# Optimization experiments

Measured on AMD Instinct MI355X. Metric: run time of the kernel, lower is better.

Reference implementation:

```python
import jax, jax.numpy as jnp
import numpy as np

K_MAX = 30


def setup_inputs() -> dict:
    key = jax.random.key(0)
    ks = jax.random.split(key, 4)
    b, N, f0, f1, f2 = 8, 256, 512, 256, 128
    x = jax.random.normal(ks[0], (b, N, f0), dtype=jnp.float32)
    W0 = jax.random.normal(ks[1], (f0, f1), dtype=jnp.float32) / np.sqrt(f0).astype(np.float32)
    b0 = jnp.zeros((f1,), jnp.float32)
    W1 = jax.random.normal(ks[2], (f1, f2), dtype=jnp.float32) / np.sqrt(f1).astype(np.float32)
    b1 = jnp.zeros((f2,), jnp.float32)
    return {"x": x, "W0": W0, "b0": b0, "W1": W1, "b1": b1}


def _dist(x, W0, b0, W1, b1):
    # DIST: 2-layer MLP (ReLU after layer 0 only), then cosine distance matrix
    h = jax.nn.relu(x @ W0 + b0)
    z = h @ W1 + b1                                   # [b,N,f2]
    corr = jnp.einsum('bnd,bmd->bnm', z, z)           # [b,N,N]
    d = jnp.diagonal(corr, axis1=1, axis2=2)          # [b,N] squared norms
    denom = jnp.sqrt(jnp.clip(d[:, :, None] * d[:, None, :], 1e-8))
    return (1.0 - corr / denom) / 2.0


def _d_sum(D):
    # D_SUM_CALC: D_sum[n,m] = sum of D over block [min(n,m)..max(n,m)]^2,
    # except the -1 subdiagonal which stays D[n, n-1] (torch code path).
    b, N, _ = D.shape
    P = jnp.pad(jnp.cumsum(jnp.cumsum(D, axis=1), axis=2), ((0, 0), (1, 0), (1, 0)))
    n = jnp.arange(N)
    lo = jnp.minimum(n[:, None], n[None, :])
    hi = jnp.maximum(n[:, None], n[None, :])
    block = P[:, hi + 1, hi + 1] - P[:, lo, hi + 1] - P[:, hi + 1, lo] + P[:, lo, lo]
    sub = (n[:, None] - n[None, :]) == 1              # row = col+1
    return jnp.where(sub, D, block)


def _c_table(D_sum, K):
    # C_TABLE_ALL: sequential DP over kk, vectorized over (nn, ii) and batch.
    b, N, _ = D_sum.shape
    nn = jnp.arange(N)[:, None]
    ii = jnp.arange(N)[None, :]
    CA0 = jnp.full((b, N, N), -1.0, dtype=D_sum.dtype).at[:, :, N - 1].set(1.0)
    C_prev = D_sum[:, :, N - 1]                       # C[:, :, 0]
    CA = [CA0]
    for kk in range(1, K):
        # temp[nn, ii] = D_sum[nn, ii] + C[ii+1, kk-1],  nn <= ii < N-kk
        Cshift = jnp.pad(C_prev[:, 1:], ((0, 0), (0, 1)))
        T = D_sum + Cshift[:, None, :]                # [b,N,N]
        valid = (ii >= nn) & (ii < N - kk)            # [N,N]
        sm = jax.nn.softmax(jnp.where(valid, -T, -1e30), axis=-1)  # softmin
        CA.append(jnp.where(valid, sm, -1.0))
        Cmin = jnp.min(jnp.where(valid, T, 1e30), axis=-1)         # [b,N]
        C_prev = jnp.where(jnp.arange(N) < N - kk, Cmin, 0.0)
    return jnp.stack(CA, axis=2)                      # [b,N,K,N]


def reference(x, W0, b0, W1, b1):
    D = _dist(x, W0, b0, W1, b1)
    Ds = _d_sum(D)
    C_all = _c_table(Ds, K_MAX)
    mask = (C_all >= 0).astype(C_all.dtype)
    return (C_all * mask).sum((1, 2)) / mask.sum((1, 2))   # [b,N]
```

## Files before the change

kernel.cpp:

```cpp
#include <hip/hip_runtime.h>

constexpr int NB    = 8;
constexpr int NN    = 256;
constexpr int F0    = 512;
constexpr int F1    = 256;
constexpr int F2    = 128;
constexpr int ROWS  = NB * NN;
constexpr int KMAX  = 30;
constexpr float INF = 1e30f;

__global__ __launch_bounds__(256) void gemm_bias_act(
    const float* __restrict__ A, const float* __restrict__ B,
    const float* __restrict__ bias, float* __restrict__ C,
    int M, int Ncols, int K, int relu)
{
  __shared__ float As[16][64];
  __shared__ float Bs[16][32];
  const int tid = threadIdx.x;
  const int tx = tid & 15;
  const int ty = tid >> 4;
  const int rowBase = blockIdx.y * 64;
  const int colBase = blockIdx.x * 32;
  float acc[4][2] = {};
  for (int k0 = 0; k0 < K; k0 += 16) {
    {
      const int r  = tid >> 2;
      const int kq = (tid & 3) << 2;
      const float4 av = *(const float4*)(A + (size_t)(rowBase + r) * K + (k0 + kq));
      As[kq+0][r] = av.x; As[kq+1][r] = av.y; As[kq+2][r] = av.z; As[kq+3][r] = av.w;
      const int kr = tid >> 4;
      const int c2 = (tid & 15) << 1;
      const float2 bv = *(const float2*)(B + (size_t)(k0 + kr) * Ncols + (colBase + c2));
      Bs[kr][c2+0] = bv.x; Bs[kr][c2+1] = bv.y;
    }
    __syncthreads();
    #pragma unroll
    for (int kk = 0; kk < 16; kk++) {
      const float4 a = *(const float4*)&As[kk][ty*4];
      const float b0v = Bs[kk][tx*2+0];
      const float b1v = Bs[kk][tx*2+1];
      acc[0][0] += a.x*b0v; acc[0][1] += a.x*b1v;
      acc[1][0] += a.y*b0v; acc[1][1] += a.y*b1v;
      acc[2][0] += a.z*b0v; acc[2][1] += a.z*b1v;
      acc[3][0] += a.w*b0v; acc[3][1] += a.w*b1v;
    }
    __syncthreads();
  }
  #pragma unroll
  for (int i = 0; i < 4; i++) {
    const int rr = rowBase + ty*4 + i;
    #pragma unroll
    for (int j = 0; j < 2; j++) {
      const int cc = colBase + tx*2 + j;
      float v = acc[i][j] + bias[cc];
      if (relu) v = fmaxf(v, 0.0f);
      C[(size_t)rr * Ncols + cc] = v;
    }
  }
}

__global__ __launch_bounds__(256) void corr_dist(
    const float* __restrict__ z, float* __restrict__ D)
{
  const int b = blockIdx.z;
  const float* zb = z + (size_t)b * NN * F2;
  __shared__ float As[16][64];
  __shared__ float Bs[16][64];
  const int tid = threadIdx.x;
  const int tx = tid & 15;
  const int ty = tid >> 4;
  const int rowBase = blockIdx.y * 64;
  const int colBase = blockIdx.x * 64;
  float acc[4][4] = {};
  float nsr[4] = {}, nsc[4] = {};
  for (int k0 = 0; k0 < F2; k0 += 16) {
    {
      const int r  = tid >> 2;
      const int kq = (tid & 3) << 2;
      const float4 av = *(const float4*)(zb + (size_t)(rowBase + r) * F2 + (k0 + kq));
      As[kq+0][r] = av.x; As[kq+1][r] = av.y; As[kq+2][r] = av.z; As[kq+3][r] = av.w;
      const float4 bv = *(const float4*)(zb + (size_t)(colBase + r) * F2 + (k0 + kq));
      Bs[kq+0][r] = bv.x; Bs[kq+1][r] = bv.y; Bs[kq+2][r] = bv.z; Bs[kq+3][r] = bv.w;
    }
    __syncthreads();
    #pragma unroll
    for (int kk = 0; kk < 16; kk++) {
      const float4 a = *(const float4*)&As[kk][ty*4];
      const float4 bq = *(const float4*)&Bs[kk][tx*4];
      const float ar[4] = {a.x, a.y, a.z, a.w};
      const float br[4] = {bq.x, bq.y, bq.z, bq.w};
      #pragma unroll
      for (int i = 0; i < 4; i++) { nsr[i] += ar[i]*ar[i]; nsc[i] += br[i]*br[i]; }
      #pragma unroll
      for (int i = 0; i < 4; i++)
        #pragma unroll
        for (int j = 0; j < 4; j++)
          acc[i][j] += ar[i] * br[j];
    }
    __syncthreads();
  }
  float* Db = D + (size_t)b * NN * NN;
  #pragma unroll
  for (int i = 0; i < 4; i++) {
    const int rr = rowBase + ty*4 + i;
    #pragma unroll
    for (int j = 0; j < 4; j++) {
      const int cc = colBase + tx*4 + j;
      const float denom = sqrtf(fmaxf(nsr[i] * nsc[j], 1e-8f));
      Db[(size_t)rr * NN + cc] = 0.5f * (1.0f - acc[i][j] / denom);
    }
  }
}

__global__ __launch_bounds__(256) void scan_slab(
    const float* __restrict__ D, double* __restrict__ S, double* __restrict__ aux)
{
  const int s = blockIdx.x & 7;
  const int b = blockIdx.x >> 3;
  const int tid = threadIdx.x;
  const int wave = tid >> 6, lane = tid & 63;
  __shared__ double sd[32][NN];
  for (int t = 0; t < 8; t++) {
    const int rl = wave * 8 + t;
    const float4 dv = *(const float4*)(D + (size_t)(b * NN + s * 32 + rl) * NN + lane * 4);
    double d0 = dv.x, d1 = dv.y, d2 = dv.z, d3 = dv.w;
    double p0 = d0, p1 = p0 + d1, p2 = p1 + d2, p3 = p2 + d3;
    double tt = p3;
    #pragma unroll
    for (int d = 1; d < 64; d <<= 1) {
      double u = __shfl_up(tt, d);
      if (lane >= d) tt += u;
    }
    const double off = tt - p3;
    sd[rl][lane*4+0] = off + p0; sd[rl][lane*4+1] = off + p1;
    sd[rl][lane*4+2] = off + p2; sd[rl][lane*4+3] = off + p3;
  }
  __syncthreads();
  const int j = tid;
  double* Sp = S + (size_t)b * NN * NN + (size_t)(s * 32) * NN + j;
  double sum = 0.0;
  for (int r = 0; r < 32; r += 8) {
    double v0 = sd[r+0][j], v1 = sd[r+1][j], v2 = sd[r+2][j], v3 = sd[r+3][j];
    double v4 = sd[r+4][j], v5 = sd[r+5][j], v6 = sd[r+6][j], v7 = sd[r+7][j];
    v0 += sum; v1 += v0; v2 += v1; v3 += v2; v4 += v3; v5 += v4; v6 += v5; v7 += v6;
    Sp[(size_t)(r+0)*NN] = v0; Sp[(size_t)(r+1)*NN] = v1;
    Sp[(size_t)(r+2)*NN] = v2; Sp[(size_t)(r+3)*NN] = v3;
    Sp[(size_t)(r+4)*NN] = v4; Sp[(size_t)(r+5)*NN] = v5;
    Sp[(size_t)(r+6)*NN] = v6; Sp[(size_t)(r+7)*NN] = v7;
    sum = v7;
  }
  aux[((size_t)b * 8 + s) * NN + j] = sum;
}

__global__ __launch_bounds__(256) void ds_mat(
    const double* __restrict__ S, const double* __restrict__ aux,
    float* __restrict__ A, float* __restrict__ Cstk, float* __restrict__ out)
{
  const int slab = blockIdx.x;
  const int b = blockIdx.y;
  const double* Sb = S + (size_t)b * NN * NN;
  float* Ab = A + (size_t)b * NN * NN;
  const int tid = threadIdx.x;
  const int w = tid >> 6, lane = tid & 63;
  __shared__ double P[8][NN];
  __shared__ double diag[NN];
  {
    const double* ax = aux + (size_t)b * 8 * NN + tid;
    double run = 0.0;
    #pragma unroll
    for (int u = 0; u < 8; u++) { P[u][tid] = run; run += ax[(size_t)u * NN]; }
  }
  __syncthreads();
  diag[tid] = Sb[(size_t)tid * NN + tid] + P[tid >> 5][tid];
  __syncthreads();
  #pragma unroll
  for (int t = 0; t < 4; t++) {
    const int n = slab * 16 + w * 4 + t;
    const double snn = (n > 0) ? diag[n-1] : 0.0;
    const double* srow = Sb + (size_t)(n > 0 ? n-1 : 0) * NN;
    const double* Pr   = P[(n > 0 ? n-1 : 0) >> 5];
    #pragma unroll
    for (int c = 0; c < 4; c++) {
      const int jx = c * 64 + lane;
      float ds = INF;
      if (jx >= n) {
        const double sv = (n > 0) ? (srow[jx] + Pr[jx]) : 0.0;
        ds = (float)(diag[jx] - 2.0 * sv + snn);
      }
      if (jx < NN - 1) Ab[(size_t)n * NN + jx + 1] = ds;
      else             Cstk[(size_t)b * 32 * NN + n] = ds;
      if (jx == 0)     Ab[(size_t)n * NN + 0] = INF;
    }
  }
  if (slab == 0) out[b * NN + tid] = (tid == NN - 1) ? 1.0f : 0.0f;
}

constexpr int CSTR = 260;
constexpr int RING = 8;

__global__ __launch_bounds__(1024) void chain_full(
    const float* __restrict__ A, float* __restrict__ Cstk)
{
  const int b = blockIdx.x;
  const int tid = threadIdx.x;
  const int n = tid >> 2, q = tid & 3;
  __shared__ __align__(16) float cs[RING * CSTR];
  float* Ck = Cstk + (size_t)b * 32 * NN;
  const size_t mb = (size_t)b * NN * NN;

  const int jj0 = (n + 1) & ~3;
  const int La  = NN - jj0;

  float4 areg[16];
  {
    const float* ar = A + mb + (size_t)n * NN + jj0;
    #pragma unroll
    for (int fi = 0; fi < 16; fi++) {
      const int f = 4 * q + 16 * fi;
      if (f < La) areg[fi] = *(const float4*)(ar + f);
      else        areg[fi] = make_float4(INF, INF, INF, INF);
    }
  }

  if (tid < NN) cs[tid] = Ck[tid];
  __syncthreads();

  for (int t = 0; t < 29; t++) {
    float m = INF;
    const float* cb = cs + (t & (RING-1)) * CSTR + jj0 + 4 * q;
    #pragma unroll
    for (int fi = 0; fi < 16; fi++) {
      const int f = 4 * q + 16 * fi;
      if (f < La) {
        const float4 a = areg[fi];
        const float4 c = *(const float4*)(cb + 16 * fi);
        m = fminf(m, fminf(fminf(a.x + c.x, a.y + c.y),
                           fminf(a.z + c.z, a.w + c.w)));
      }
    }
    m = fminf(m, __shfl_xor(m, 1));
    m = fminf(m, __shfl_xor(m, 2));
    m = fminf(m, INF);
    if (q == 0) {
      cs[((t + 1) & (RING-1)) * CSTR + n] = m;
      Ck[(t + 1) * NN + n] = m;
    }
    __syncthreads();
  }
}

__global__ __launch_bounds__(256) void sm_fused(
    const float* __restrict__ A, const float* __restrict__ Cstk,
    float* __restrict__ out)
{
  const int k = blockIdx.x + 1;
  const int b = blockIdx.y;
  const int limit = NN - k;
  const int tid = threadIdx.x;
  const float* Ab  = A + (size_t)b * NN * NN;
  const float* Ckb = Cstk + (size_t)b * 32 * NN;
  __shared__ __align__(16) float cprev[NN];
  __shared__ float ck[NN];
  __shared__ float ivh[NN];
  cprev[tid] = Ckb[(k - 1) * NN + tid];
  ck[tid]    = Ckb[k * NN + tid];
  __syncthreads();
  const int r = tid >> 2, q = tid & 3;
  #pragma unroll
  for (int rg = 0; rg < 4; rg++) {
    const int n = rg * 64 + r;
    const float m = ck[n];
    const float* Ar = Ab + (size_t)n * NN + q * 64;
    float s = 0.f;
    if (q * 64 + 63 > n) {
      #pragma unroll 4
      for (int i = 0; i < 16; i++) {
        const float4 a = *(const float4*)(Ar + i * 4);
        const int jj = q * 64 + i * 4;
        const float4 c = *(const float4*)&cprev[jj];
        s += (jj + 0 <= limit) ? __expf(m - a.x - c.x) : 0.f;
        s += (jj + 1 <= limit) ? __expf(m - a.y - c.y) : 0.f;
        s += (jj + 2 <= limit) ? __expf(m - a.z - c.z) : 0.f;
        s += (jj + 3 <= limit) ? __expf(m - a.w - c.w) : 0.f;
      }
    }
    s += __shfl_xor(s, 1);
    s += __shfl_xor(s, 2);
    if (q == 0) ivh[n] = 1.0f / s;
  }
  __syncthreads();
  const int j = tid;
  if (j < limit) {
    const float cj = cprev[j + 1];
    const int nmax = (j < limit - 1) ? j : limit - 1;
    float a = 0.0f;
    #pragma unroll 4
    for (int nr = 0; nr <= nmax; nr++)
      a += __expf(ck[nr] - Ab[(size_t)nr * NN + j + 1] - cj) * ivh[nr];
    int kmaxj = NN - 1 - j; if (kmaxj > KMAX - 1) kmaxj = KMAX - 1;
    const float cnt = (float)((j + 1) * kmaxj);
    atomicAdd(&out[b * NN + j], a / cnt);
  }
}

extern "C" void kernel_launch(void* const* d_in, const int* in_sizes, int n_in,
                              void* d_out, int out_size, void* d_ws, size_t ws_size,
                              hipStream_t stream) {
  const float* x  = (const float*)d_in[0];
  const float* W0 = (const float*)d_in[1];
  const float* b0 = (const float*)d_in[2];
  const float* W1 = (const float*)d_in[3];
  const float* b1 = (const float*)d_in[4];
  float* out = (float*)d_out;

  char* base = (char*)d_ws;
  float*  h    = (float*)(base);
  double* S    = (double*)(base);
  float*  D    = (float*)(base + (4u << 20));
  float*  A    = (float*)(base + (4u << 20));
  float*  z    = (float*)(base + (6u << 20));
  float*  Cstk = (float*)(base + (6u << 20));
  double* aux  = (double*)(base + (7u << 20));

  gemm_bias_act<<<dim3(F1/32, ROWS/64), 256, 0, stream>>>(x, W0, b0, h, ROWS, F1, F0, 1);
  gemm_bias_act<<<dim3(F2/32, ROWS/64), 256, 0, stream>>>(h, W1, b1, z, ROWS, F2, F1, 0);
  corr_dist<<<dim3(NN/64, NN/64, NB), 256, 0, stream>>>(z, D);
  scan_slab<<<dim3(NB*8), 256, 0, stream>>>(D, S, aux);
  ds_mat<<<dim3(16, NB), 256, 0, stream>>>(S, aux, A, Cstk, out);
  chain_full<<<dim3(NB), 1024, 0, stream>>>(A, Cstk);
  sm_fused<<<dim3(KMAX-1, NB), 256, 0, stream>>>(A, Cstk, out);
}
```

Baseline: 186.1 us.

## Fuse D_sum matrix construction into the DP chain kernel

Merges the ds_mat kernel into chain_full so each of the 8 batch blocks computes its own D_sum row entries from the prefix-sum data straight into registers, and still writes A out for the later softmin kernel. This drops one launch and the global round-trip that reloaded A before the DP. In exchange, the D_sum work runs on only 8 blocks instead of 128, so that part gets much less parallelism, and the scattered double-precision loads from S now happen inside the serial kernel.

New measurement: 209.1 us. 1.12x slower.

```diff
diff --git a/kernel.cpp b/kernel.cpp
--- a/kernel.cpp
+++ b/kernel.cpp
@@ -152,77 +152,67 @@
   aux[((size_t)b * 8 + s) * NN + j] = sum;
 }
 
-__global__ __launch_bounds__(256) void ds_mat(
+constexpr int CSTR = 260;
+constexpr int RING = 8;
+
+__global__ __launch_bounds__(1024) void ds_chain(
     const double* __restrict__ S, const double* __restrict__ aux,
     float* __restrict__ A, float* __restrict__ Cstk, float* __restrict__ out)
 {
-  const int slab = blockIdx.x;
-  const int b = blockIdx.y;
+  const int b = blockIdx.x;
+  const int tid = threadIdx.x;
+  const int n = tid >> 2, q = tid & 3;
+  __shared__ double P[8][NN];
+  __shared__ double diag[NN];
+  __shared__ __align__(16) float cs[RING * CSTR];
   const double* Sb = S + (size_t)b * NN * NN;
   float* Ab = A + (size_t)b * NN * NN;
-  const int tid = threadIdx.x;
-  const int w = tid >> 6, lane = tid & 63;
-  __shared__ double P[8][NN];
-  __shared__ double diag[NN];
-  {
+  float* Ck = Cstk + (size_t)b * 32 * NN;
+
+  if (tid < NN) {
     const double* ax = aux + (size_t)b * 8 * NN + tid;
     double run = 0.0;
     #pragma unroll
     for (int u = 0; u < 8; u++) { P[u][tid] = run; run += ax[(size_t)u * NN]; }
   }
   __syncthreads();
-  diag[tid] = Sb[(size_t)tid * NN + tid] + P[tid >> 5][tid];
-  __syncthreads();
-  #pragma unroll
-  for (int t = 0; t < 4; t++) {
-    const int n = slab * 16 + w * 4 + t;
-    const double snn = (n > 0) ? diag[n-1] : 0.0;
-    const double* srow = Sb + (size_t)(n > 0 ? n-1 : 0) * NN;
-    const double* Pr   = P[(n > 0 ? n-1 : 0) >> 5];
-    #pragma unroll
-    for (int c = 0; c < 4; c++) {
-      const int jx = c * 64 + lane;
-      float ds = INF;
-      if (jx >= n) {
-        const double sv = (n > 0) ? (srow[jx] + Pr[jx]) : 0.0;
-        ds = (float)(diag[jx] - 2.0 * sv + snn);
-      }
-      if (jx < NN - 1) Ab[(size_t)n * NN + jx + 1] = ds;
-      else             Cstk[(size_t)b * 32 * NN + n] = ds;
-      if (jx == 0)     Ab[(size_t)n * NN + 0] = INF;
-    }
-  }
-  if (slab == 0) out[b * NN + tid] = (tid == NN - 1) ? 1.0f : 0.0f;
-}
-
-constexpr int CSTR = 260;
-constexpr int RING = 8;
-
-__global__ __launch_bounds__(1024) void chain_full(
-    const float* __restrict__ A, float* __restrict__ Cstk)
-{
-  const int b = blockIdx.x;
-  const int tid = threadIdx.x;
-  const int n = tid >> 2, q = tid & 3;
-  __shared__ __align__(16) float cs[RING * CSTR];
-  float* Ck = Cstk + (size_t)b * 32 * NN;
-  const size_t mb = (size_t)b * NN * NN;
+  if (tid < NN) diag[tid] = Sb[(size_t)tid * NN + tid] + P[tid >> 5][tid];
+  __syncthreads();
 
   const int jj0 = (n + 1) & ~3;
   const int La  = NN - jj0;
+  const double snn = (n > 0) ? diag[n-1] : 0.0;
+  const double* srow = Sb + (size_t)(n > 0 ? n-1 : 0) * NN;
+  const double* Pr   = P[(n > 0 ? n-1 : 0) >> 5];
 
   float4 areg[16];
-  {
-    const float* ar = A + mb + (size_t)n * NN + jj0;
-    #pragma unroll
-    for (int fi = 0; fi < 16; fi++) {
-      const int f = 4 * q + 16 * fi;
-      if (f < La) areg[fi] = *(const float4*)(ar + f);
-      else        areg[fi] = make_float4(INF, INF, INF, INF);
-    }
-  }
-
-  if (tid < NN) cs[tid] = Ck[tid];
+  #pragma unroll
+  for (int fi = 0; fi < 16; fi++) {
+    const int f = 4 * q + 16 * fi;
+    if (f < La) {
+      float v[4];
+      #pragma unroll
+      for (int c = 0; c < 4; c++) {
+        const int col = jj0 + f + c;
+        if (col > n) {
+          const int jx = col - 1;
+          const double sv = (n > 0) ? (srow[jx] + Pr[jx]) : 0.0;
+          v[c] = (float)(diag[jx] - 2.0 * sv + snn);
+        } else v[c] = INF;
+      }
+      areg[fi] = make_float4(v[0], v[1], v[2], v[3]);
+      *(float4*)(Ab + (size_t)n * NN + jj0 + f) = areg[fi];
+    } else areg[fi] = make_float4(INF, INF, INF, INF);
+  }
+  for (int c4 = q; c4 < (jj0 >> 2); c4 += 4)
+    *(float4*)(Ab + (size_t)n * NN + 4 * c4) = make_float4(INF, INF, INF, INF);
+  if (q == 0) {
+    const double sv = (n > 0) ? (srow[NN-1] + Pr[NN-1]) : 0.0;
+    const float c0 = (float)(diag[NN-1] - 2.0 * sv + snn);
+    cs[n] = c0;
+    Ck[n] = c0;
+  }
+  if (tid < NN) out[b * NN + tid] = (tid == NN - 1) ? 1.0f : 0.0f;
   __syncthreads();
 
   for (int t = 0; t < 29; t++) {
@@ -326,7 +316,6 @@
   gemm_bias_act<<<dim3(F2/32, ROWS/64), 256, 0, stream>>>(h, W1, b1, z, ROWS, F2, F1, 0);
   corr_dist<<<dim3(NN/64, NN/64, NB), 256, 0, stream>>>(z, D);
   scan_slab<<<dim3(NB*8), 256, 0, stream>>>(D, S, aux);
-  ds_mat<<<dim3(16, NB), 256, 0, stream>>>(S, aux, A, Cstk, out);
-  chain_full<<<dim3(NB), 1024, 0, stream>>>(A, Cstk);
+  ds_chain<<<dim3(NB), 1024, 0, stream>>>(S, aux, A, Cstk, out);
   sm_fused<<<dim3(KMAX-1, NB), 256, 0, stream>>>(A, Cstk, out);
 }
```
